# Kernel tuning notes

Hardware: AMD Instinct MI355X
Metric: run time of the kernel (lower is better)

## Reference

```python
import jax, jax.numpy as jnp
import numpy as np

N, H = 131072, 256          # rows, hidden_dim
P, K_OCC, K_SUBJ = 16, 8, 16  # phases, occurrences per phase, subjects per occurrence
O = P * K_OCC               # 128 total occurrence classes
S = O * K_SUBJ              # 2048 total subject classes


def setup_inputs() -> dict:
    key = jax.random.key(0)
    ks = jax.random.split(key, 10)
    X = jax.random.normal(ks[0], (N, H), jnp.float32)
    X_phase = jax.random.randint(ks[1], (N,), 0, P)
    X_occ_local = jax.random.randint(ks[2], (N,), 0, K_OCC)
    X_subj_local = jax.random.randint(ks[3], (N,), 0, K_SUBJ)
    sc = 1.0 / np.sqrt(H)  # nn.Linear default init range
    W_phase = jax.random.uniform(ks[4], (P, H), jnp.float32, -sc, sc)
    b_phase = jax.random.uniform(ks[5], (P,), jnp.float32, -sc, sc)
    W_p2o = jax.random.uniform(ks[6], (O, H), jnp.float32, -sc, sc)      # stacked phase_to_occurrence Linears
    b_p2o = jax.random.uniform(ks[7], (O,), jnp.float32, -sc, sc)
    W_o2s = jax.random.uniform(ks[8], (S, H), jnp.float32, -sc, sc)      # stacked occurrence_to_subj Linears
    b_o2s = jax.random.uniform(ks[9], (S,), jnp.float32, -sc, sc)
    return {
        "X": X, "W_phase": W_phase, "b_phase": b_phase,
        "W_p2o": W_p2o, "b_p2o": b_p2o, "W_o2s": W_o2s, "b_o2s": b_o2s,
        "X_phase": X_phase, "X_occ_local": X_occ_local, "X_subj_local": X_subj_local,
    }


def reference(X, W_phase, b_phase, W_p2o, b_p2o, W_o2s, b_o2s,
              X_phase, X_occ_local, X_subj_local):
    n = X.shape[0]
    rows = jnp.arange(n)

    # phase head: softmax over all P phases, pick the true phase prob
    phase_proba = jax.nn.softmax(X @ W_phase.T + b_phase, axis=1)[rows, X_phase]  # [N]

    # occurrence head: per-sample small Linear chosen by phase key -> compute all
    # stacked logits once, gather the phase's K_OCC-block, softmax within block
    occ_logits = (X @ W_p2o.T + b_p2o).reshape(n, P, K_OCC)[rows, X_phase]        # [N, K_OCC]
    occ_proba = jax.nn.softmax(occ_logits, axis=1)[rows, X_occ_local]             # [N]

    # subject head: same pattern keyed by global occurrence id
    X_occurrence = X_phase * K_OCC + X_occ_local                                   # global occ ids
    subj_logits = (X @ W_o2s.T + b_o2s).reshape(n, O, K_SUBJ)[rows, X_occurrence]  # [N, K_SUBJ]
    subj_proba = jax.nn.softmax(subj_logits, axis=1)[rows, X_subj_local]           # [N]

    po = phase_proba * occ_proba
    return (phase_proba, po, po * subj_proba)
```

## Files before the change

kernel.cpp:

```cpp
#include <hip/hip_runtime.h>

#define H_ 256
#define P_ 16
#define KOCC 8
#define KSUBJ 16
#define O_ 128
#define CAPMAX 2048

typedef __attribute__((ext_vector_type(8))) __bf16 bf16x8;
typedef __attribute__((ext_vector_type(4))) float f32x4;

__device__ __forceinline__ bf16x8 load_bf8(const float* p) {
  float4 a = *(const float4*)p;
  float4 b = *(const float4*)(p + 4);
  bf16x8 r;
  r[0] = (__bf16)a.x; r[1] = (__bf16)a.y; r[2] = (__bf16)a.z; r[3] = (__bf16)a.w;
  r[4] = (__bf16)b.x; r[5] = (__bf16)b.y; r[6] = (__bf16)b.z; r[7] = (__bf16)b.w;
  return r;
}

__device__ __forceinline__ bf16x8 cvt_bf8(float4 a, float4 b) {
  bf16x8 r;
  r[0] = (__bf16)a.x; r[1] = (__bf16)a.y; r[2] = (__bf16)a.z; r[3] = (__bf16)a.w;
  r[4] = (__bf16)b.x; r[5] = (__bf16)b.y; r[6] = (__bf16)b.z; r[7] = (__bf16)b.w;
  return r;
}

__device__ __forceinline__ float rsum16(float v) {
  v += __shfl_xor(v, 1);
  v += __shfl_xor(v, 2);
  v += __shfl_xor(v, 4);
  v += __shfl_xor(v, 8);
  return v;
}

__global__ __launch_bounds__(1024) void scatter_kernel(
    const int* __restrict__ xp, const int* __restrict__ xo,
    int* counts, int* brows, int n, int cap) {
  __shared__ int hist[O_];
  __shared__ int basev[O_];
  int tid = threadIdx.x;
  if (tid < O_) hist[tid] = 0;
  __syncthreads();
  int base_i = blockIdx.x * 4096 + tid;
  int be[4], pos[4];
#pragma unroll
  for (int e = 0; e < 4; ++e) {
    int i = base_i + e * 1024;
    pos[e] = -1;
    if (i < n) {
      be[e] = xp[i] * KOCC + xo[i];
      pos[e] = atomicAdd(&hist[be[e]], 1);
    }
  }
  __syncthreads();
  if (tid < O_) basev[tid] = atomicAdd(&counts[tid], hist[tid]);
  __syncthreads();
#pragma unroll
  for (int e = 0; e < 4; ++e) {
    if (pos[e] >= 0) {
      int idx = basev[be[e]] + pos[e];
      if (idx < cap) brows[be[e] * cap + idx] = base_i + e * 1024;
    }
  }
}

__global__ __launch_bounds__(256) void hsm_main(
    const float* __restrict__ X,
    const float* __restrict__ Wp, const float* __restrict__ bp,
    const float* __restrict__ Wo, const float* __restrict__ bo,
    const float* __restrict__ Ws, const float* __restrict__ bs,
    const int* __restrict__ subj,
    const int* __restrict__ counts, const int* __restrict__ brows,
    float* __restrict__ out, int n, int cap) {
  int b = blockIdx.x & 127;
  int chunk = blockIdx.x >> 7;
  int count = counts[b];
  if (count > cap) count = cap;
  int p = b >> 3;
  int occl = b & 7;

  __shared__ __bf16 Bf[3 * 8 * 64 * 8];
  {
    int t = threadIdx.x;
#pragma unroll
    for (int it = 0; it < 6; ++it) {
      int fid = it * 256 + t;
      int lane_f = fid & 63;
      int hk = fid >> 6;
      int head = hk >> 3, kk = hk & 7;
      int colf = lane_f & 15, quadf = lane_f >> 4;
      const float* src;
      if (head == 0)      src = Wp + colf * H_;
      else if (head == 1) src = Wo + (p * KOCC + (colf & 7)) * H_;
      else                src = Ws + (b * KSUBJ + colf) * H_;
      bf16x8 v = load_bf8(src + kk * 32 + quadf * 8);
      *(bf16x8*)&Bf[(size_t)fid * 8] = v;
    }
  }
  __syncthreads();

  int lane = threadIdx.x & 63;
  int wave = threadIdx.x >> 6;
  int col = lane & 15;
  int quad = lane >> 4;

  bool v1 = col < KOCC;
  float bias0 = bp[col];
  float bias1 = v1 ? bo[p * KOCC + col] : 0.0f;
  float bias2 = bs[b * KSUBJ + col];

  const int* brow_b = brows + b * cap;
  const bf16x8* Bfrag = (const bf16x8*)Bf;

  for (int base = chunk * 64 + wave * 16; base < count; base += 1024) {
    int rem = count - base;
    int rida = brow_b[base + (col < rem ? col : rem - 1)];
    int subjv = subj[rida];
    const float* xr = X + (size_t)rida * H_;

    float4 ta[8], tb[8];
#pragma unroll
    for (int kk = 0; kk < 8; ++kk) {
      const float4* src = (const float4*)(xr + kk * 32 + quad * 8);
      ta[kk] = src[0];
      tb[kk] = src[1];
    }
    __builtin_amdgcn_sched_barrier(0);

    f32x4 acc0 = {0.f, 0.f, 0.f, 0.f};
    f32x4 acc1 = {0.f, 0.f, 0.f, 0.f};
    f32x4 acc2 = {0.f, 0.f, 0.f, 0.f};
#pragma unroll
    for (int kk = 0; kk < 8; ++kk) {
      bf16x8 a = cvt_bf8(ta[kk], tb[kk]);
      acc0 = __builtin_amdgcn_mfma_f32_16x16x32_bf16(a, Bfrag[kk * 64 + lane], acc0, 0, 0, 0);
      acc1 = __builtin_amdgcn_mfma_f32_16x16x32_bf16(a, Bfrag[(8 + kk) * 64 + lane], acc1, 0, 0, 0);
      acc2 = __builtin_amdgcn_mfma_f32_16x16x32_bf16(a, Bfrag[(16 + kk) * 64 + lane], acc2, 0, 0, 0);
    }

#pragma unroll
    for (int r = 0; r < 4; ++r) {
      int rloc = quad * 4 + r;
      bool rv = rloc < rem;
      int ridr = __shfl(rida, rloc);
      int tsub = __shfl(subjv, rloc);
      float e0 = __expf(acc0[r] + bias0);
      float s0 = rsum16(e0);
      float p0 = __shfl(e0, quad * 16 + p) / s0;
      float e1 = v1 ? __expf(acc1[r] + bias1) : 0.0f;
      float s1 = rsum16(e1);
      float p1 = __shfl(e1, quad * 16 + occl) / s1;
      float e2 = __expf(acc2[r] + bias2);
      float s2 = rsum16(e2);
      float p2 = __shfl(e2, quad * 16 + tsub) / s2;
      if (col == 0 && rv) {
        float po = p0 * p1;
        out[ridr] = p0;
        out[n + ridr] = po;
        out[2 * n + ridr] = po * p2;
      }
    }
  }
}

extern "C" void kernel_launch(void* const* d_in, const int* in_sizes, int n_in,
                              void* d_out, int out_size, void* d_ws, size_t ws_size,
                              hipStream_t stream) {
  const float* X  = (const float*)d_in[0];
  const float* Wp = (const float*)d_in[1];
  const float* bp = (const float*)d_in[2];
  const float* Wo = (const float*)d_in[3];
  const float* bo = (const float*)d_in[4];
  const float* Ws = (const float*)d_in[5];
  const float* bs = (const float*)d_in[6];
  const int* xp   = (const int*)d_in[7];
  const int* xo   = (const int*)d_in[8];
  const int* xs   = (const int*)d_in[9];
  float* out = (float*)d_out;
  int n = in_sizes[7];

  int* wsI = (int*)d_ws;
  int* counts = wsI;
  int* brows = wsI + 128;
  long avail = (long)(ws_size / 4) - 128;
  int cap = (int)(avail / O_);
  if (cap > CAPMAX) cap = CAPMAX;
  if (cap < 1) cap = 1;

  hipMemsetAsync(counts, 0, O_ * sizeof(int), stream);
  scatter_kernel<<<dim3((n + 4095) / 4096), dim3(1024), 0, stream>>>(xp, xo, counts, brows, n, cap);
  hsm_main<<<dim3(O_ * 16), dim3(256), 0, stream>>>(X, Wp, bp, Wo, bo, Ws, bs, xs,
                                                    counts, brows, out, n, cap);
}
```

Measured before the change: 223.1 us.

## Double-buffer X row loads across groups and shrink grid to four chunks per bucket

The main loop is split into issue and process helpers. The next 16-row group's X loads are issued before the current group's MFMA and softmax run, using two register buffers in ping-pong fashion. The grid drops from 16 to 4 chunks per bucket, so each wave handles several groups in sequence, and launch bounds now request 2 blocks per CU. This is meant to hide global-load latency through software prefetch. The cost is fewer resident waves and higher register pressure from the doubled load buffers.

Measured after the change: 221.1 us. Within noise of the previous version (-0.9%).

```diff
diff --git a/kernel.cpp b/kernel.cpp
--- a/kernel.cpp
+++ b/kernel.cpp
@@ -65,7 +65,62 @@
   }
 }
 
-__global__ __launch_bounds__(256) void hsm_main(
+__device__ __forceinline__ void issue_group(
+    const int* __restrict__ brow_b, const int* __restrict__ subj,
+    const float* __restrict__ X, int base, int count, int col, int quad,
+    int& rida, int& subjv, int& rem, float4* ta, float4* tb) {
+  rem = count - base;
+  rida = brow_b[base + (col < rem ? col : rem - 1)];
+  subjv = subj[rida];
+  const float* xr = X + (size_t)rida * H_ + quad * 8;
+#pragma unroll
+  for (int kk = 0; kk < 8; ++kk) {
+    const float4* s = (const float4*)(xr + kk * 32);
+    ta[kk] = s[0];
+    tb[kk] = s[1];
+  }
+}
+
+__device__ __forceinline__ void process_group(
+    const bf16x8* __restrict__ Bfrag, int lane, int col, int quad,
+    int p, int occl, bool v1, float bias0, float bias1, float bias2,
+    int rida, int subjv, int rem, const float4* ta, const float4* tb,
+    float* __restrict__ out, int n) {
+  f32x4 acc0 = {0.f, 0.f, 0.f, 0.f};
+  f32x4 acc1 = {0.f, 0.f, 0.f, 0.f};
+  f32x4 acc2 = {0.f, 0.f, 0.f, 0.f};
+#pragma unroll
+  for (int kk = 0; kk < 8; ++kk) {
+    bf16x8 a = cvt_bf8(ta[kk], tb[kk]);
+    acc0 = __builtin_amdgcn_mfma_f32_16x16x32_bf16(a, Bfrag[kk * 64 + lane], acc0, 0, 0, 0);
+    acc1 = __builtin_amdgcn_mfma_f32_16x16x32_bf16(a, Bfrag[(8 + kk) * 64 + lane], acc1, 0, 0, 0);
+    acc2 = __builtin_amdgcn_mfma_f32_16x16x32_bf16(a, Bfrag[(16 + kk) * 64 + lane], acc2, 0, 0, 0);
+  }
+#pragma unroll
+  for (int r = 0; r < 4; ++r) {
+    int rloc = quad * 4 + r;
+    bool rv = rloc < rem;
+    int ridr = __shfl(rida, rloc);
+    int tsub = __shfl(subjv, rloc);
+    float e0 = __expf(acc0[r] + bias0);
+    float s0 = rsum16(e0);
+    float p0 = __shfl(e0, quad * 16 + p) / s0;
+    float e1 = v1 ? __expf(acc1[r] + bias1) : 0.0f;
+    float s1 = rsum16(e1);
+    float p1 = __shfl(e1, quad * 16 + occl) / s1;
+    float e2 = __expf(acc2[r] + bias2);
+    float s2 = rsum16(e2);
+    float p2 = __shfl(e2, quad * 16 + tsub) / s2;
+    if (col == 0 && rv) {
+      float po = p0 * p1;
+      out[ridr] = p0;
+      out[n + ridr] = po;
+      out[2 * n + ridr] = po * p2;
+    }
+  }
+}
+
+__global__ __launch_bounds__(256, 2) void hsm_main(
     const float* __restrict__ X,
     const float* __restrict__ Wp, const float* __restrict__ bp,
     const float* __restrict__ Wo, const float* __restrict__ bo,
@@ -113,54 +168,28 @@
   const int* brow_b = brows + b * cap;
   const bf16x8* Bfrag = (const bf16x8*)Bf;
 
-  for (int base = chunk * 64 + wave * 16; base < count; base += 1024) {
-    int rem = count - base;
-    int rida = brow_b[base + (col < rem ? col : rem - 1)];
-    int subjv = subj[rida];
-    const float* xr = X + (size_t)rida * H_;
-
-    float4 ta[8], tb[8];
-#pragma unroll
-    for (int kk = 0; kk < 8; ++kk) {
-      const float4* src = (const float4*)(xr + kk * 32 + quad * 8);
-      ta[kk] = src[0];
-      tb[kk] = src[1];
-    }
+  int base = chunk * 64 + wave * 16;
+  if (base >= count) return;
+
+  float4 taA[8], tbA[8], taB[8], tbB[8];
+  int ridaA, subjA, remA, ridaB, subjB, remB;
+  issue_group(brow_b, subj, X, base, count, col, quad, ridaA, subjA, remA, taA, tbA);
+  while (true) {
+    bool vB = (base + 256) < count;
+    if (vB)
+      issue_group(brow_b, subj, X, base + 256, count, col, quad, ridaB, subjB, remB, taB, tbB);
     __builtin_amdgcn_sched_barrier(0);
-
-    f32x4 acc0 = {0.f, 0.f, 0.f, 0.f};
-    f32x4 acc1 = {0.f, 0.f, 0.f, 0.f};
-    f32x4 acc2 = {0.f, 0.f, 0.f, 0.f};
-#pragma unroll
-    for (int kk = 0; kk < 8; ++kk) {
-      bf16x8 a = cvt_bf8(ta[kk], tb[kk]);
-      acc0 = __builtin_amdgcn_mfma_f32_16x16x32_bf16(a, Bfrag[kk * 64 + lane], acc0, 0, 0, 0);
-      acc1 = __builtin_amdgcn_mfma_f32_16x16x32_bf16(a, Bfrag[(8 + kk) * 64 + lane], acc1, 0, 0, 0);
-      acc2 = __builtin_amdgcn_mfma_f32_16x16x32_bf16(a, Bfrag[(16 + kk) * 64 + lane], acc2, 0, 0, 0);
-    }
-
-#pragma unroll
-    for (int r = 0; r < 4; ++r) {
-      int rloc = quad * 4 + r;
-      bool rv = rloc < rem;
-      int ridr = __shfl(rida, rloc);
-      int tsub = __shfl(subjv, rloc);
-      float e0 = __expf(acc0[r] + bias0);
-      float s0 = rsum16(e0);
-      float p0 = __shfl(e0, quad * 16 + p) / s0;
-      float e1 = v1 ? __expf(acc1[r] + bias1) : 0.0f;
-      float s1 = rsum16(e1);
-      float p1 = __shfl(e1, quad * 16 + occl) / s1;
-      float e2 = __expf(acc2[r] + bias2);
-      float s2 = rsum16(e2);
-      float p2 = __shfl(e2, quad * 16 + tsub) / s2;
-      if (col == 0 && rv) {
-        float po = p0 * p1;
-        out[ridr] = p0;
-        out[n + ridr] = po;
-        out[2 * n + ridr] = po * p2;
-      }
-    }
+    process_group(Bfrag, lane, col, quad, p, occl, v1, bias0, bias1, bias2,
+                  ridaA, subjA, remA, taA, tbA, out, n);
+    if (!vB) break;
+    bool vA2 = (base + 512) < count;
+    if (vA2)
+      issue_group(brow_b, subj, X, base + 512, count, col, quad, ridaA, subjA, remA, taA, tbA);
+    __builtin_amdgcn_sched_barrier(0);
+    process_group(Bfrag, lane, col, quad, p, occl, v1, bias0, bias1, bias2,
+                  ridaB, subjB, remB, taB, tbB, out, n);
+    if (!vA2) break;
+    base += 512;
   }
 }
 
@@ -190,6 +219,6 @@
 
   hipMemsetAsync(counts, 0, O_ * sizeof(int), stream);
   scatter_kernel<<<dim3((n + 4095) / 4096), dim3(1024), 0, stream>>>(xp, xo, counts, brows, n, cap);
-  hsm_main<<<dim3(O_ * 16), dim3(256), 0, stream>>>(X, Wp, bp, Wo, bo, Ws, bs, xs,
-                                                    counts, brows, out, n, cap);
-}
+  hsm_main<<<dim3(O_ * 4), dim3(256), 0, stream>>>(X, Wp, bp, Wo, bo, Ws, bs, xs,
+                                                   counts, brows, out, n, cap);
+}
```
